# Kernel tuning notes

Hardware: AMD Instinct MI355X
Metric: run time of the kernel (lower is better)

## Reference

```python
import jax, jax.numpy as jnp
import numpy as np

# Model hyperparameters (match init_kwargs)
NUM_HEADS = 12
KEY_SIZE = 64
VALUE_SIZE = 64
D_MODEL = 768
NUM_LAYERS = 4
FFW = 3072
B, T, L = 2, 32, 256
LN_EPS = 1e-5


def _layer_norm(x, scale, offset):
    m = jnp.mean(x, axis=-1, keepdims=True)
    v = jnp.mean(jnp.square(x - m), axis=-1, keepdims=True)
    return (x - m) * jax.lax.rsqrt(v + LN_EPS) * scale + offset


def _axial_attn(x, Wq, Wk, Wv, Wo, bo, mode):
    # x: [B, T, L, D]
    b, t, l, d = x.shape
    q = (x @ Wq).reshape(b, t, l, NUM_HEADS, KEY_SIZE)
    k = (x @ Wk).reshape(b, t, l, NUM_HEADS, KEY_SIZE)
    v = (x @ Wv).reshape(b, t, l, NUM_HEADS, VALUE_SIZE)
    inv_sqrt_d = KEY_SIZE ** (-0.5)
    if mode == 'time':
        logits = jnp.einsum('btlhd,bTlhd->blhtT', q, k) * inv_sqrt_d
        w = jax.nn.softmax(logits, axis=-1)
        a = jnp.einsum('blhtT,bTlhd->btlhd', w, v)
    else:  # space
        logits = jnp.einsum('btlhd,btLhd->bthlL', q, k) * inv_sqrt_d
        w = jax.nn.softmax(logits, axis=-1)
        a = jnp.einsum('bthlL,btLhd->btlhd', w, v)
    a = a.reshape(b, t, l, NUM_HEADS * VALUE_SIZE)
    return a @ Wo + bo


def _forward(input_embeddings, Wq_t, Wk_t, Wv_t, Wo_t, bo_t,
             Wq_s, Wk_s, Wv_s, Wo_s, bo_s,
             ln_t_scale, ln_t_bias, ln_s_scale, ln_s_bias,
             ln2_scale, ln2_bias, W1, b1, W2, b2):
    def block(h, p):
        (wq_t, wk_t, wv_t, wo_t, bot, wq_s, wk_s, wv_s, wo_s, bos,
         lts, ltb, lss, lsb, l2s, l2b, w1, bb1, w2, bb2) = p
        # time attention + residual
        x = _layer_norm(h, lts, ltb)
        h = h + _axial_attn(x, wq_t, wk_t, wv_t, wo_t, bot, 'time')
        # space attention + residual
        x = _layer_norm(h, lss, lsb)
        h = h + _axial_attn(x, wq_s, wk_s, wv_s, wo_s, bos, 'space')
        # FFN + residual
        x = _layer_norm(h, l2s, l2b)
        ff = jax.nn.gelu(x @ w1 + bb1) @ w2 + bb2
        return h + ff, None

    params = (Wq_t, Wk_t, Wv_t, Wo_t, bo_t, Wq_s, Wk_s, Wv_s, Wo_s, bo_s,
              ln_t_scale, ln_t_bias, ln_s_scale, ln_s_bias,
              ln2_scale, ln2_bias, W1, b1, W2, b2)
    h, _ = jax.lax.scan(block, input_embeddings, params)
    return h


def setup_inputs() -> dict:
    key = jax.random.key(0)
    ks = jax.random.split(key, 32)
    D, H, KD, VD, F, NL = D_MODEL, NUM_HEADS, KEY_SIZE, VALUE_SIZE, FFW, NUM_LAYERS
    init_scale = 2.0 / np.sqrt(NL)  # VarianceScaling scale used by the module
    s_in = np.sqrt(init_scale / D).astype(np.float32)   # fan_in = D
    s_out = np.sqrt(init_scale / (H * VD)).astype(np.float32)
    s_ffw2 = np.sqrt(init_scale / F).astype(np.float32)
    x = jax.random.normal(ks[0], (B, T, L, D), dtype=jnp.float32)
    def nrm(k, shape, s):
        return jax.random.normal(k, shape, dtype=jnp.float32) * s
    inp = {
        'input_embeddings': x,
        'Wq_t': nrm(ks[1], (NL, D, H * KD), s_in),
        'Wk_t': nrm(ks[2], (NL, D, H * KD), s_in),
        'Wv_t': nrm(ks[3], (NL, D, H * VD), s_in),
        'Wo_t': nrm(ks[4], (NL, H * VD, D), s_out),
        'bo_t': jnp.zeros((NL, D), jnp.float32),
        'Wq_s': nrm(ks[5], (NL, D, H * KD), s_in),
        'Wk_s': nrm(ks[6], (NL, D, H * KD), s_in),
        'Wv_s': nrm(ks[7], (NL, D, H * VD), s_in),
        'Wo_s': nrm(ks[8], (NL, H * VD, D), s_out),
        'bo_s': jnp.zeros((NL, D), jnp.float32),
        'ln_t_scale': jnp.ones((NL, D), jnp.float32),
        'ln_t_bias': jnp.zeros((NL, D), jnp.float32),
        'ln_s_scale': jnp.ones((NL, D), jnp.float32),
        'ln_s_bias': jnp.zeros((NL, D), jnp.float32),
        'ln2_scale': jnp.ones((NL, D), jnp.float32),
        'ln2_bias': jnp.zeros((NL, D), jnp.float32),
        'W1': nrm(ks[9], (NL, D, F), s_in),
        'b1': jnp.zeros((NL, F), jnp.float32),
        'W2': nrm(ks[10], (NL, F, D), s_ffw2),
        'b2': jnp.zeros((NL, D), jnp.float32),
    }
    return inp


def reference(input_embeddings, Wq_t, Wk_t, Wv_t, Wo_t, bo_t,
              Wq_s, Wk_s, Wv_s, Wo_s, bo_s,
              ln_t_scale, ln_t_bias, ln_s_scale, ln_s_bias,
              ln2_scale, ln2_bias, W1, b1, W2, b2):
    return _forward(input_embeddings, Wq_t, Wk_t, Wv_t, Wo_t, bo_t,
                    Wq_s, Wk_s, Wv_s, Wo_s, bo_s,
                    ln_t_scale, ln_t_bias, ln_s_scale, ln_s_bias,
                    ln2_scale, ln2_bias, W1, b1, W2, b2)
```

## Files before the change

### kernel.cpp

```cpp
#include <hip/hip_runtime.h>


#define AS1 __attribute__((address_space(1)))
#define AS3 __attribute__((address_space(3)))

using bf16x8 = __attribute__((ext_vector_type(8))) short;
using f32x4  = __attribute__((ext_vector_type(4))) float;

__device__ __forceinline__ f32x4 mfma_bf16(bf16x8 a, bf16x8 b, f32x4 c) {
  return __builtin_amdgcn_mfma_f32_16x16x32_bf16(a, b, c, 0, 0, 0);
}

__device__ __forceinline__ void async16(const void* g, void* l) {
  __builtin_amdgcn_global_load_lds((const AS1 void*)g, (AS3 void*)l, 16, 0, 0);
}

__device__ __forceinline__ short f2bs(float f) {
  union { float f; unsigned u; } x; x.f = f;
  unsigned r = x.u + 0x7fffu + ((x.u >> 16) & 1u);
  return (short)(r >> 16);
}

__device__ __forceinline__ f32x4 fzero() {
  f32x4 v; v[0] = 0.f; v[1] = 0.f; v[2] = 0.f; v[3] = 0.f; return v;
}

__device__ __forceinline__ float quad16_max(float v) {
  v = fmaxf(v, __shfl_xor(v, 1));
  v = fmaxf(v, __shfl_xor(v, 2));
  v = fmaxf(v, __shfl_xor(v, 4));
  v = fmaxf(v, __shfl_xor(v, 8));
  return v;
}
__device__ __forceinline__ float quad16_sum(float v) {
  v += __shfl_xor(v, 1); v += __shfl_xor(v, 2);
  v += __shfl_xor(v, 4); v += __shfl_xor(v, 8);
  return v;
}

template<int MODE>
__global__ __launch_bounds__(256) void gemm_bt(
    const short* __restrict__ A, const short* __restrict__ BT,
    const float* __restrict__ bias, const float* __restrict__ resid,
    float* __restrict__ outF, short* __restrict__ outB,
    int M, int N, int K, int nx)
{
  __shared__ __align__(16) short lA[128 * 64];
  __shared__ __align__(16) short lB[128 * 64];
  const int tid  = threadIdx.x;
  const int wave = tid >> 6, lane = tid & 63;
  const int quad = lane >> 4, l16 = lane & 15;
  const int wm = wave >> 1, wn = wave & 1;

  const unsigned flat = blockIdx.x;
  const unsigned su = flat >> 3;
  const unsigned nxu = (unsigned)nx;
  const unsigned xt = su % nxu;
  const unsigned yt = (flat & 7u) + 8u * (su / nxu);
  const long bm0 = (long)yt * 128;
  const long bn0 = (long)xt * 128;

  const int srow = lane >> 3;
  const int skof = ((lane & 7) ^ srow) * 8;

  f32x4 acc[4][4];
#pragma unroll
  for (int i = 0; i < 4; ++i)
#pragma unroll
    for (int j = 0; j < 4; ++j) acc[i][j] = fzero();

  for (int k0 = 0; k0 < K; k0 += 64) {
    __syncthreads();
#pragma unroll
    for (int cc = 0; cc < 4; ++cc) {
      int c = wave * 4 + cc;
      long row = c * 8 + srow;
      async16(A  + (bm0 + row) * (long)K + k0 + skof, (char*)lA + c * 1024);
      async16(BT + (bn0 + row) * (long)K + k0 + skof, (char*)lB + c * 1024);
    }
    __syncthreads();
#pragma unroll
    for (int kk = 0; kk < 2; ++kk) {
      bf16x8 a[4], b[4];
      const int pg = ((kk * 4 + quad) ^ (l16 & 7)) * 8;
#pragma unroll
      for (int i = 0; i < 4; ++i)
        a[i] = *(const bf16x8*)&lA[(wm * 64 + i * 16 + l16) * 64 + pg];
#pragma unroll
      for (int j = 0; j < 4; ++j)
        b[j] = *(const bf16x8*)&lB[(wn * 64 + j * 16 + l16) * 64 + pg];
#pragma unroll
      for (int i = 0; i < 4; ++i)
#pragma unroll
        for (int j = 0; j < 4; ++j)
          acc[i][j] = mfma_bf16(a[i], b[j], acc[i][j]);
    }
  }

#pragma unroll
  for (int i = 0; i < 4; ++i)
#pragma unroll
    for (int j = 0; j < 4; ++j)
#pragma unroll
      for (int r = 0; r < 4; ++r) {
        long gr = bm0 + wm * 64 + i * 16 + quad * 4 + r;
        long gc = bn0 + wn * 64 + j * 16 + l16;
        size_t idx = (size_t)gr * N + gc;
        float v = acc[i][j][r];
        if (MODE == 0) {
          outB[idx] = f2bs(v);
        } else if (MODE == 1) {
          outF[idx] = v + bias[gc] + resid[idx];
        } else {
          float t = v + bias[gc];
          float g = 0.5f * t * (1.f + tanhf(0.7978845608f * (t + 0.044715f * t * t * t)));
          outB[idx] = f2bs(g);
        }
      }
}

__global__ __launch_bounds__(256) void ln_kernel(
    const float* __restrict__ h, const float* __restrict__ sc,
    const float* __restrict__ bi, short* __restrict__ out)
{
  const int row = blockIdx.x, tid = threadIdx.x;
  const float* hr = h + (long)row * 768;
  float x0 = hr[tid], x1 = hr[tid + 256], x2 = hr[tid + 512];
  __shared__ float red[4];
  float s = x0 + x1 + x2;
#pragma unroll
  for (int m = 32; m >= 1; m >>= 1) s += __shfl_xor(s, m);
  if ((tid & 63) == 0) red[tid >> 6] = s;
  __syncthreads();
  float mean = (red[0] + red[1] + red[2] + red[3]) * (1.f / 768.f);
  float d0 = x0 - mean, d1 = x1 - mean, d2 = x2 - mean;
  float q = d0 * d0 + d1 * d1 + d2 * d2;
#pragma unroll
  for (int m = 32; m >= 1; m >>= 1) q += __shfl_xor(q, m);
  __syncthreads();
  if ((tid & 63) == 0) red[tid >> 6] = q;
  __syncthreads();
  float var = (red[0] + red[1] + red[2] + red[3]) * (1.f / 768.f);
  float inv = rsqrtf(var + 1e-5f);
  long o = (long)row * 768;
  out[o + tid]       = f2bs(d0 * inv * sc[tid]       + bi[tid]);
  out[o + tid + 256] = f2bs(d1 * inv * sc[tid + 256] + bi[tid + 256]);
  out[o + tid + 512] = f2bs(d2 * inv * sc[tid + 512] + bi[tid + 512]);
}

__global__ __launch_bounds__(256) void transpose_w(
    const float* __restrict__ in, short* __restrict__ out, int Kd, int Nd)
{
  __shared__ float t[32][33];
  const int n0 = blockIdx.x * 32, k0 = blockIdx.y * 32;
  const int r = threadIdx.x >> 5, c = threadIdx.x & 31;
#pragma unroll
  for (int rr = 0; rr < 4; ++rr)
    t[r + rr * 8][c] = in[(long)(k0 + r + rr * 8) * Nd + n0 + c];
  __syncthreads();
#pragma unroll
  for (int rr = 0; rr < 4; ++rr)
    out[(long)(n0 + r + rr * 8) * Kd + k0 + c] = f2bs(t[c][r + rr * 8]);
}

__global__ __launch_bounds__(256) void attn_space(
    const short* __restrict__ qkv, short* __restrict__ ao)
{
  __shared__ __align__(16) short VT[64 * 256];
  __shared__ __align__(16) short P[4][16 * 256];
  const int qt = blockIdx.x, hh = blockIdx.y, bt = blockIdx.z;
  const long tok0 = (long)bt * 256;
  const int tid = threadIdx.x, wave = tid >> 6, lane = tid & 63;
  const int quad = lane >> 4, l16 = lane & 15;

#pragma unroll
  for (int it = 0; it < 8; ++it) {
    int chunk = it * 256 + tid;
    int vl = chunk >> 3, d8 = (chunk & 7) * 8;
    bf16x8 v = *(const bf16x8*)(qkv + (tok0 + vl) * 2304 + 1536 + hh * 64 + d8);
#pragma unroll
    for (int e = 0; e < 8; ++e) VT[(d8 + e) * 256 + vl] = v[e];
  }

  const int qr = qt * 64 + wave * 16;
  bf16x8 qf[2];
#pragma unroll
  for (int kk = 0; kk < 2; ++kk)
    qf[kk] = *(const bf16x8*)(qkv + (tok0 + qr + l16) * 2304 + hh * 64 + kk * 32 + quad * 8);

  f32x4 S[16];
#pragma unroll
  for (int j = 0; j < 16; ++j) S[j] = fzero();
#pragma unroll
  for (int j = 0; j < 16; ++j)
#pragma unroll
    for (int kk = 0; kk < 2; ++kk) {
      bf16x8 kf = *(const bf16x8*)(qkv + (tok0 + j * 16 + l16) * 2304 + 768 + hh * 64 + kk * 32 + quad * 8);
      S[j] = mfma_bf16(qf[kk], kf, S[j]);
    }

#pragma unroll
  for (int r = 0; r < 4; ++r) {
    float m = -1e30f;
#pragma unroll
    for (int j = 0; j < 16; ++j) m = fmaxf(m, S[j][r]);
    m = quad16_max(m);
    float sum = 0.f;
#pragma unroll
    for (int j = 0; j < 16; ++j) {
      float e = __expf((S[j][r] - m) * 0.125f);
      S[j][r] = e; sum += e;
    }
    sum = quad16_sum(sum);
    float inv = 1.f / sum;
#pragma unroll
    for (int j = 0; j < 16; ++j)
      P[wave][(quad * 4 + r) * 256 + j * 16 + l16] = f2bs(S[j][r] * inv);
  }
  __syncthreads();

  f32x4 O[4];
#pragma unroll
  for (int jn = 0; jn < 4; ++jn) O[jn] = fzero();
  for (int kk = 0; kk < 8; ++kk) {
    bf16x8 pf = *(const bf16x8*)&P[wave][l16 * 256 + kk * 32 + quad * 8];
#pragma unroll
    for (int jn = 0; jn < 4; ++jn) {
      bf16x8 vf = *(const bf16x8*)&VT[(jn * 16 + l16) * 256 + kk * 32 + quad * 8];
      O[jn] = mfma_bf16(pf, vf, O[jn]);
    }
  }
#pragma unroll
  for (int jn = 0; jn < 4; ++jn)
#pragma unroll
    for (int r = 0; r < 4; ++r) {
      int row = qr + quad * 4 + r;
      ao[(tok0 + row) * 768 + hh * 64 + jn * 16 + l16] = f2bs(O[jn][r]);
    }
}

__global__ __launch_bounds__(64) void attn_time(
    const short* __restrict__ qkv, short* __restrict__ ao)
{
  __shared__ __align__(16) short VT[64 * 32];
  __shared__ __align__(16) short P[32 * 32];
  const int ll = blockIdx.x, hh = blockIdx.y, b = blockIdx.z;
  const int lane = threadIdx.x;
  const int quad = lane >> 4, l16 = lane & 15;
#define TOK(t) (((long)(b * 32 + (t))) * 256 + ll)

#pragma unroll
  for (int it = 0; it < 4; ++it) {
    int chunk = it * 64 + lane;
    int t = chunk >> 3, d8 = (chunk & 7) * 8;
    bf16x8 v = *(const bf16x8*)(qkv + TOK(t) * 2304 + 1536 + hh * 64 + d8);
#pragma unroll
    for (int e = 0; e < 8; ++e) VT[(d8 + e) * 32 + t] = v[e];
  }

  bf16x8 qf[2][2];
#pragma unroll
  for (int mi = 0; mi < 2; ++mi)
#pragma unroll
    for (int kk = 0; kk < 2; ++kk)
      qf[mi][kk] = *(const bf16x8*)(qkv + TOK(mi * 16 + l16) * 2304 + hh * 64 + kk * 32 + quad * 8);

  f32x4 S[2][2];
#pragma unroll
  for (int mi = 0; mi < 2; ++mi) { S[mi][0] = fzero(); S[mi][1] = fzero(); }
#pragma unroll
  for (int nj = 0; nj < 2; ++nj)
#pragma unroll
    for (int kk = 0; kk < 2; ++kk) {
      bf16x8 kf = *(const bf16x8*)(qkv + TOK(nj * 16 + l16) * 2304 + 768 + hh * 64 + kk * 32 + quad * 8);
#pragma unroll
      for (int mi = 0; mi < 2; ++mi)
        S[mi][nj] = mfma_bf16(qf[mi][kk], kf, S[mi][nj]);
    }

#pragma unroll
  for (int mi = 0; mi < 2; ++mi)
#pragma unroll
    for (int r = 0; r < 4; ++r) {
      float m = fmaxf(S[mi][0][r], S[mi][1][r]);
      m = quad16_max(m);
      float e0 = __expf((S[mi][0][r] - m) * 0.125f);
      float e1 = __expf((S[mi][1][r] - m) * 0.125f);
      float sum = quad16_sum(e0 + e1);
      float inv = 1.f / sum;
      P[(mi * 16 + quad * 4 + r) * 32 + l16]      = f2bs(e0 * inv);
      P[(mi * 16 + quad * 4 + r) * 32 + 16 + l16] = f2bs(e1 * inv);
    }
  __syncthreads();

  f32x4 O[2][4];
#pragma unroll
  for (int mi = 0; mi < 2; ++mi)
#pragma unroll
    for (int jn = 0; jn < 4; ++jn) O[mi][jn] = fzero();
#pragma unroll
  for (int mi = 0; mi < 2; ++mi) {
    bf16x8 pf = *(const bf16x8*)&P[(mi * 16 + l16) * 32 + quad * 8];
#pragma unroll
    for (int jn = 0; jn < 4; ++jn) {
      bf16x8 vf = *(const bf16x8*)&VT[(jn * 16 + l16) * 32 + quad * 8];
      O[mi][jn] = mfma_bf16(pf, vf, O[mi][jn]);
    }
  }
#pragma unroll
  for (int mi = 0; mi < 2; ++mi)
#pragma unroll
    for (int jn = 0; jn < 4; ++jn)
#pragma unroll
      for (int r = 0; r < 4; ++r) {
        int t = mi * 16 + quad * 4 + r;
        ao[TOK(t) * 768 + hh * 64 + jn * 16 + l16] = f2bs(O[mi][jn][r]);
      }
#undef TOK
}

extern "C" void kernel_launch(void* const* d_in, const int* in_sizes, int n_in,
                              void* d_out, int out_size, void* d_ws, size_t ws_size,
                              hipStream_t stream)
{
  const float* emb     = (const float*)d_in[0];
  const float* Wq_t    = (const float*)d_in[1];
  const float* Wk_t    = (const float*)d_in[2];
  const float* Wv_t    = (const float*)d_in[3];
  const float* Wo_t    = (const float*)d_in[4];
  const float* bo_t    = (const float*)d_in[5];
  const float* Wq_s    = (const float*)d_in[6];
  const float* Wk_s    = (const float*)d_in[7];
  const float* Wv_s    = (const float*)d_in[8];
  const float* Wo_s    = (const float*)d_in[9];
  const float* bo_s    = (const float*)d_in[10];
  const float* ln_t_sc = (const float*)d_in[11];
  const float* ln_t_bi = (const float*)d_in[12];
  const float* ln_s_sc = (const float*)d_in[13];
  const float* ln_s_bi = (const float*)d_in[14];
  const float* ln2_sc  = (const float*)d_in[15];
  const float* ln2_bi  = (const float*)d_in[16];
  const float* W1      = (const float*)d_in[17];
  const float* b1      = (const float*)d_in[18];
  const float* W2      = (const float*)d_in[19];
  const float* b2      = (const float*)d_in[20];

  const long M = 16384, D = 768, QN = 2304, F = 3072;
  char* ws = (char*)d_ws;
  size_t off = 0;
  auto alloc = [&](size_t b) { char* p = ws + off; off += (b + 255) & ~(size_t)255; return p; };
  short* qkvT_t = (short*)alloc((size_t)4 * QN * D * 2);
  short* qkvT_s = (short*)alloc((size_t)4 * QN * D * 2);
  short* woT_t  = (short*)alloc((size_t)4 * D * D * 2);
  short* woT_s  = (short*)alloc((size_t)4 * D * D * 2);
  short* w1T    = (short*)alloc((size_t)4 * F * D * 2);
  short* w2T    = (short*)alloc((size_t)4 * D * F * 2);
  short* xb     = (short*)alloc((size_t)M * D * 2);
  short* aob    = (short*)alloc((size_t)M * D * 2);
  short* big    = (short*)alloc((size_t)M * F * 2);
  float* h = (float*)d_out;

  hipMemcpyAsync(h, emb, (size_t)M * D * 4, hipMemcpyDeviceToDevice, stream);

  for (int l = 0; l < 4; ++l) {
    const long wo = (long)l * D * D;
    transpose_w<<<dim3(24, 24), 256, 0, stream>>>(Wq_t + wo, qkvT_t + (long)l * QN * D,            768, 768);
    transpose_w<<<dim3(24, 24), 256, 0, stream>>>(Wk_t + wo, qkvT_t + (long)l * QN * D + D * D,    768, 768);
    transpose_w<<<dim3(24, 24), 256, 0, stream>>>(Wv_t + wo, qkvT_t + (long)l * QN * D + 2 * D * D, 768, 768);
    transpose_w<<<dim3(24, 24), 256, 0, stream>>>(Wq_s + wo, qkvT_s + (long)l * QN * D,            768, 768);
    transpose_w<<<dim3(24, 24), 256, 0, stream>>>(Wk_s + wo, qkvT_s + (long)l * QN * D + D * D,    768, 768);
    transpose_w<<<dim3(24, 24), 256, 0, stream>>>(Wv_s + wo, qkvT_s + (long)l * QN * D + 2 * D * D, 768, 768);
    transpose_w<<<dim3(24, 24), 256, 0, stream>>>(Wo_t + wo, woT_t + wo, 768, 768);
    transpose_w<<<dim3(24, 24), 256, 0, stream>>>(Wo_s + wo, woT_s + wo, 768, 768);
    transpose_w<<<dim3(96, 24), 256, 0, stream>>>(W1 + (long)l * D * F, w1T + (long)l * F * D, 768, 3072);
    transpose_w<<<dim3(24, 96), 256, 0, stream>>>(W2 + (long)l * F * D, w2T + (long)l * D * F, 3072, 768);
  }

  for (int l = 0; l < 4; ++l) {
    ln_kernel<<<16384, 256, 0, stream>>>(h, ln_t_sc + l * 768, ln_t_bi + l * 768, xb);
    gemm_bt<0><<<18 * 128, 256, 0, stream>>>(xb, qkvT_t + (long)l * QN * D,
        nullptr, nullptr, nullptr, big, 16384, 2304, 768, 18);
    attn_time<<<dim3(256, 12, 2), 64, 0, stream>>>(big, aob);
    gemm_bt<1><<<6 * 128, 256, 0, stream>>>(aob, woT_t + (long)l * D * D,
        bo_t + l * 768, h, h, nullptr, 16384, 768, 768, 6);
    ln_kernel<<<16384, 256, 0, stream>>>(h, ln_s_sc + l * 768, ln_s_bi + l * 768, xb);
    gemm_bt<0><<<18 * 128, 256, 0, stream>>>(xb, qkvT_s + (long)l * QN * D,
        nullptr, nullptr, nullptr, big, 16384, 2304, 768, 18);
    attn_space<<<dim3(4, 12, 64), 256, 0, stream>>>(big, aob);
    gemm_bt<1><<<6 * 128, 256, 0, stream>>>(aob, woT_s + (long)l * D * D,
        bo_s + l * 768, h, h, nullptr, 16384, 768, 768, 6);
    ln_kernel<<<16384, 256, 0, stream>>>(h, ln2_sc + l * 768, ln2_bi + l * 768, xb);
    gemm_bt<2><<<24 * 128, 256, 0, stream>>>(xb, w1T + (long)l * F * D,
        b1 + l * 3072, nullptr, nullptr, big, 16384, 3072, 768, 24);
    gemm_bt<1><<<6 * 128, 256, 0, stream>>>(big, w2T + (long)l * D * F,
        b2 + l * 768, h, h, nullptr, 16384, 768, 3072, 6);
  }
}
```

Measured before the change: 2.799 ms.

## Replace GEMM with 256x256 tiled, 4-stage async pipelined kernel; batch weight transposes

Replaces the 128x128 single-buffered GEMM with a 512-thread 256x256-tile kernel. It uses a 4-deep ring of async global-to-LDS loads with explicit vmcnt waits, a new XOR swizzle, and setprio around the MFMA block. The aim is to hide global load latency and raise data reuse per tile. The 40 per-layer weight transpose launches are also folded into 10 launches using a z grid dimension. The trade-offs are higher register and LDS use (128KB LDS per block, so likely one block per CU) and fewer blocks for the N=768 GEMMs (192 blocks).

```diff
diff --git a/kernel.cpp b/kernel.cpp
--- a/kernel.cpp
+++ b/kernel.cpp
@@ -39,84 +39,122 @@
 }
 
 template<int MODE>
-__global__ __launch_bounds__(256) void gemm_bt(
+__global__ __launch_bounds__(512, 2) void gemm256(
     const short* __restrict__ A, const short* __restrict__ BT,
     const float* __restrict__ bias, const float* __restrict__ resid,
     float* __restrict__ outF, short* __restrict__ outB,
     int M, int N, int K, int nx)
 {
-  __shared__ __align__(16) short lA[128 * 64];
-  __shared__ __align__(16) short lB[128 * 64];
+  __shared__ __align__(16) short lds[65536];
+  (void)M;
   const int tid  = threadIdx.x;
   const int wave = tid >> 6, lane = tid & 63;
   const int quad = lane >> 4, l16 = lane & 15;
-  const int wm = wave >> 1, wn = wave & 1;
+  const int wm = wave >> 2, wn = wave & 3;
 
   const unsigned flat = blockIdx.x;
   const unsigned su = flat >> 3;
   const unsigned nxu = (unsigned)nx;
-  const unsigned xt = su % nxu;
-  const unsigned yt = (flat & 7u) + 8u * (su / nxu);
-  const long bm0 = (long)yt * 128;
-  const long bn0 = (long)xt * 128;
-
-  const int srow = lane >> 3;
-  const int skof = ((lane & 7) ^ srow) * 8;
-
-  f32x4 acc[4][4];
-#pragma unroll
-  for (int i = 0; i < 4; ++i)
+  const long bm0 = (long)((flat & 7u) + 8u * (su / nxu)) * 256;
+  const long bn0 = (long)(su % nxu) * 256;
+
+  const int srow = lane >> 2;
+  const int skof = ((lane & 3) ^ ((lane >> 3) & 3)) * 8;
+  const int r0 = wave * 32;
+  const short* gA0 = A  + (bm0 + r0 + srow) * (long)K + skof;
+  const short* gA1 = gA0 + 16 * (long)K;
+  const short* gB0 = BT + (bn0 + r0 + srow) * (long)K + skof;
+  const short* gB1 = gB0 + 16 * (long)K;
+  char* const lbase = (char*)lds;
+  const int dA0 = r0 * 64, dA1 = (r0 + 16) * 64;
+  const int dB0 = 16384 + r0 * 64, dB1 = 16384 + (r0 + 16) * 64;
+
+  int aoff[8], boff[4];
+#pragma unroll
+  for (int i = 0; i < 8; ++i) {
+    int row = wm * 128 + i * 16 + l16;
+    aoff[i] = row * 32 + (quad ^ ((row >> 1) & 3)) * 8;
+  }
+#pragma unroll
+  for (int j = 0; j < 4; ++j) {
+    int row = wn * 64 + j * 16 + l16;
+    boff[j] = 8192 + row * 32 + (quad ^ ((row >> 1) & 3)) * 8;
+  }
+
+  f32x4 acc[8][4];
+#pragma unroll
+  for (int i = 0; i < 8; ++i)
 #pragma unroll
     for (int j = 0; j < 4; ++j) acc[i][j] = fzero();
 
-  for (int k0 = 0; k0 < K; k0 += 64) {
-    __syncthreads();
-#pragma unroll
-    for (int cc = 0; cc < 4; ++cc) {
-      int c = wave * 4 + cc;
-      long row = c * 8 + srow;
-      async16(A  + (bm0 + row) * (long)K + k0 + skof, (char*)lA + c * 1024);
-      async16(BT + (bn0 + row) * (long)K + k0 + skof, (char*)lB + c * 1024);
-    }
-    __syncthreads();
-#pragma unroll
-    for (int kk = 0; kk < 2; ++kk) {
-      bf16x8 a[4], b[4];
-      const int pg = ((kk * 4 + quad) ^ (l16 & 7)) * 8;
-#pragma unroll
-      for (int i = 0; i < 4; ++i)
-        a[i] = *(const bf16x8*)&lA[(wm * 64 + i * 16 + l16) * 64 + pg];
+  const int nt = K >> 5;
+
+#define STAGE(t)                                                         \
+  do {                                                                   \
+    const int sb_ = ((t) & 3) * 32768;                                   \
+    const long ko_ = (long)(t) * 32;                                     \
+    async16(gA0 + ko_, lbase + sb_ + dA0);                               \
+    async16(gA1 + ko_, lbase + sb_ + dA1);                               \
+    async16(gB0 + ko_, lbase + sb_ + dB0);                               \
+    async16(gB1 + ko_, lbase + sb_ + dB1);                               \
+  } while (0)
+
+  STAGE(0); STAGE(1); STAGE(2);
+
+  for (int t = 0; t < nt; ++t) {
+    if (t + 3 < nt) STAGE(t + 3);
+    const int ahead = nt - 1 - t;
+    if (ahead >= 3)      asm volatile("s_waitcnt vmcnt(12)" ::: "memory");
+    else if (ahead == 2) asm volatile("s_waitcnt vmcnt(8)"  ::: "memory");
+    else if (ahead == 1) asm volatile("s_waitcnt vmcnt(4)"  ::: "memory");
+    else                 asm volatile("s_waitcnt vmcnt(0)"  ::: "memory");
+    __builtin_amdgcn_s_barrier();
+    asm volatile("" ::: "memory");
+    __builtin_amdgcn_sched_barrier(0);
+
+    const short* sbase = lds + (t & 3) * 16384;
+    bf16x8 a[8], b[4];
+#pragma unroll
+    for (int i = 0; i < 8; ++i) a[i] = *(const bf16x8*)(sbase + aoff[i]);
+#pragma unroll
+    for (int j = 0; j < 4; ++j) b[j] = *(const bf16x8*)(sbase + boff[j]);
+    asm volatile("s_waitcnt lgkmcnt(0)" ::: "memory");
+    __builtin_amdgcn_sched_barrier(0);
+    __builtin_amdgcn_s_barrier();
+
+    __builtin_amdgcn_s_setprio(1);
+#pragma unroll
+    for (int i = 0; i < 8; ++i)
 #pragma unroll
       for (int j = 0; j < 4; ++j)
-        b[j] = *(const bf16x8*)&lB[(wn * 64 + j * 16 + l16) * 64 + pg];
-#pragma unroll
-      for (int i = 0; i < 4; ++i)
-#pragma unroll
-        for (int j = 0; j < 4; ++j)
-          acc[i][j] = mfma_bf16(a[i], b[j], acc[i][j]);
-    }
-  }
-
-#pragma unroll
-  for (int i = 0; i < 4; ++i)
-#pragma unroll
-    for (int j = 0; j < 4; ++j)
+        acc[i][j] = mfma_bf16(a[i], b[j], acc[i][j]);
+    __builtin_amdgcn_s_setprio(0);
+  }
+#undef STAGE
+
+  const long rowbase = bm0 + wm * 128 + quad * 4;
+  const long colbase = bn0 + wn * 64 + l16;
+#pragma unroll
+  for (int i = 0; i < 8; ++i)
+#pragma unroll
+    for (int j = 0; j < 4; ++j) {
+      const long gc = colbase + j * 16;
 #pragma unroll
       for (int r = 0; r < 4; ++r) {
-        long gr = bm0 + wm * 64 + i * 16 + quad * 4 + r;
-        long gc = bn0 + wn * 64 + j * 16 + l16;
-        size_t idx = (size_t)gr * N + gc;
+        const long gr = rowbase + i * 16 + r;
+        const size_t idx = (size_t)gr * N + gc;
         float v = acc[i][j][r];
         if (MODE == 0) {
           outB[idx] = f2bs(v);
         } else if (MODE == 1) {
           outF[idx] = v + bias[gc] + resid[idx];
         } else {
-          float t = v + bias[gc];
-          float g = 0.5f * t * (1.f + tanhf(0.7978845608f * (t + 0.044715f * t * t * t)));
+          float tt = v + bias[gc];
+          float g = 0.5f * tt * (1.f + tanhf(0.7978845608f * (tt + 0.044715f * tt * tt * tt)));
           outB[idx] = f2bs(g);
         }
       }
+    }
 }
 
 __global__ __launch_bounds__(256) void ln_kernel(
@@ -149,9 +187,13 @@
 }
 
 __global__ __launch_bounds__(256) void transpose_w(
-    const float* __restrict__ in, short* __restrict__ out, int Kd, int Nd)
+    const float* __restrict__ in, short* __restrict__ out, int Kd, int Nd,
+    long inStride, long outStride)
 {
   __shared__ float t[32][33];
+  const int z = blockIdx.z;
+  in  += (long)z * inStride;
+  out += (long)z * outStride;
   const int n0 = blockIdx.x * 32, k0 = blockIdx.y * 32;
   const int r = threadIdx.x >> 5, c = threadIdx.x & 31;
 #pragma unroll
@@ -362,37 +404,34 @@
 
   hipMemcpyAsync(h, emb, (size_t)M * D * 4, hipMemcpyDeviceToDevice, stream);
 
-  for (int l = 0; l < 4; ++l) {
-    const long wo = (long)l * D * D;
-    transpose_w<<<dim3(24, 24), 256, 0, stream>>>(Wq_t + wo, qkvT_t + (long)l * QN * D,            768, 768);
-    transpose_w<<<dim3(24, 24), 256, 0, stream>>>(Wk_t + wo, qkvT_t + (long)l * QN * D + D * D,    768, 768);
-    transpose_w<<<dim3(24, 24), 256, 0, stream>>>(Wv_t + wo, qkvT_t + (long)l * QN * D + 2 * D * D, 768, 768);
-    transpose_w<<<dim3(24, 24), 256, 0, stream>>>(Wq_s + wo, qkvT_s + (long)l * QN * D,            768, 768);
-    transpose_w<<<dim3(24, 24), 256, 0, stream>>>(Wk_s + wo, qkvT_s + (long)l * QN * D + D * D,    768, 768);
-    transpose_w<<<dim3(24, 24), 256, 0, stream>>>(Wv_s + wo, qkvT_s + (long)l * QN * D + 2 * D * D, 768, 768);
-    transpose_w<<<dim3(24, 24), 256, 0, stream>>>(Wo_t + wo, woT_t + wo, 768, 768);
-    transpose_w<<<dim3(24, 24), 256, 0, stream>>>(Wo_s + wo, woT_s + wo, 768, 768);
-    transpose_w<<<dim3(96, 24), 256, 0, stream>>>(W1 + (long)l * D * F, w1T + (long)l * F * D, 768, 3072);
-    transpose_w<<<dim3(24, 96), 256, 0, stream>>>(W2 + (long)l * F * D, w2T + (long)l * D * F, 3072, 768);
-  }
+  transpose_w<<<dim3(24, 24, 4), 256, 0, stream>>>(Wq_t, qkvT_t,             768, 768,  D * D, QN * D);
+  transpose_w<<<dim3(24, 24, 4), 256, 0, stream>>>(Wk_t, qkvT_t + D * D,     768, 768,  D * D, QN * D);
+  transpose_w<<<dim3(24, 24, 4), 256, 0, stream>>>(Wv_t, qkvT_t + 2 * D * D, 768, 768,  D * D, QN * D);
+  transpose_w<<<dim3(24, 24, 4), 256, 0, stream>>>(Wq_s, qkvT_s,             768, 768,  D * D, QN * D);
+  transpose_w<<<dim3(24, 24, 4), 256, 0, stream>>>(Wk_s, qkvT_s + D * D,     768, 768,  D * D, QN * D);
+  transpose_w<<<dim3(24, 24, 4), 256, 0, stream>>>(Wv_s, qkvT_s + 2 * D * D, 768, 768,  D * D, QN * D);
+  transpose_w<<<dim3(24, 24, 4), 256, 0, stream>>>(Wo_t, woT_t,              768, 768,  D * D, D * D);
+  transpose_w<<<dim3(24, 24, 4), 256, 0, stream>>>(Wo_s, woT_s,              768, 768,  D * D, D * D);
+  transpose_w<<<dim3(96, 24, 4), 256, 0, stream>>>(W1,   w1T,                768, 3072, D * F, F * D);
+  transpose_w<<<dim3(24, 96, 4), 256, 0, stream>>>(W2,   w2T,                3072, 768, F * D, D * F);
 
   for (int l = 0; l < 4; ++l) {
     ln_kernel<<<16384, 256, 0, stream>>>(h, ln_t_sc + l * 768, ln_t_bi + l * 768, xb);
-    gemm_bt<0><<<18 * 128, 256, 0, stream>>>(xb, qkvT_t + (long)l * QN * D,
-        nullptr, nullptr, nullptr, big, 16384, 2304, 768, 18);
+    gemm256<0><<<9 * 64, 512, 0, stream>>>(xb, qkvT_t + (long)l * QN * D,
+        nullptr, nullptr, nullptr, big, 16384, 2304, 768, 9);
     attn_time<<<dim3(256, 12, 2), 64, 0, stream>>>(big, aob);
-    gemm_bt<1><<<6 * 128, 256, 0, stream>>>(aob, woT_t + (long)l * D * D,
-        bo_t + l * 768, h, h, nullptr, 16384, 768, 768, 6);
+    gemm256<1><<<3 * 64, 512, 0, stream>>>(aob, woT_t + (long)l * D * D,
+        bo_t + l * 768, h, h, nullptr, 16384, 768, 768, 3);
     ln_kernel<<<16384, 256, 0, stream>>>(h, ln_s_sc + l * 768, ln_s_bi + l * 768, xb);
-    gemm_bt<0><<<18 * 128, 256, 0, stream>>>(xb, qkvT_s + (long)l * QN * D,
-        nullptr, nullptr, nullptr, big, 16384, 2304, 768, 18);
+    gemm256<0><<<9 * 64, 512, 0, stream>>>(xb, qkvT_s + (long)l * QN * D,
+        nullptr, nullptr, nullptr, big, 16384, 2304, 768, 9);
     attn_space<<<dim3(4, 12, 64), 256, 0, stream>>>(big, aob);
-    gemm_bt<1><<<6 * 128, 256, 0, stream>>>(aob, woT_s + (long)l * D * D,
-        bo_s + l * 768, h, h, nullptr, 16384, 768, 768, 6);
+    gemm256<1><<<3 * 64, 512, 0, stream>>>(aob, woT_s + (long)l * D * D,
+        bo_s + l * 768, h, h, nullptr, 16384, 768, 768, 3);
     ln_kernel<<<16384, 256, 0, stream>>>(h, ln2_sc + l * 768, ln2_bi + l * 768, xb);
-    gemm_bt<2><<<24 * 128, 256, 0, stream>>>(xb, w1T + (long)l * F * D,
-        b1 + l * 3072, nullptr, nullptr, big, 16384, 3072, 768, 24);
-    gemm_bt<1><<<6 * 128, 256, 0, stream>>>(big, w2T + (long)l * D * F,
-        b2 + l * 768, h, h, nullptr, 16384, 768, 3072, 6);
-  }
-}
+    gemm256<2><<<12 * 64, 512, 0, stream>>>(xb, w1T + (long)l * F * D,
+        b1 + l * 3072, nullptr, nullptr, big, 16384, 3072, 768, 12);
+    gemm256<1><<<3 * 64, 512, 0, stream>>>(big, w2T + (long)l * D * F,
+        b2 + l * 768, h, h, nullptr, 16384, 768, 3072, 3);
+  }
+}
```

New measurement: 2.733 ms. 2.4% less time.
